# Performance work log

Hardware: AMD Instinct MI355X
Metric: run time of the kernel (lower is better)

The kernel has to match this reference:

```python
import jax, jax.numpy as jnp
import numpy as np

B, S, D = 2, 2048, 1024
H, DH = 16, 64  # num_heads, per-head depth (kd//H == vd//H)
NEG = -1e10


def setup_inputs() -> dict:
    key = jax.random.key(0)
    ks = jax.random.split(key, 5)
    scale = 0.02
    return {
        "X": jax.random.normal(ks[0], (B, S, D), dtype=jnp.float32),
        "Wq": jax.random.normal(ks[1], (D, D), dtype=jnp.float32) * scale,
        "Wk": jax.random.normal(ks[2], (D, D), dtype=jnp.float32) * scale,
        "Wv": jax.random.normal(ks[3], (D, D), dtype=jnp.float32) * scale,
        "Wo": jax.random.normal(ks[4], (D, D), dtype=jnp.float32) * scale,
    }


def reference(X, Wq, Wk, Wv, Wo):
    # torch nn.Linear(in,out,bias=False): y = x @ W.T, W is [out,in]
    q = X @ Wq.T  # [B,S,H*DH]
    k = X @ Wk.T
    v = X @ Wv.T
    # split heads -> [B,H,S,DH]
    q = q.reshape(B, S, H, DH).transpose(0, 2, 1, 3) * (DH ** -0.5)
    k = k.reshape(B, S, H, DH).transpose(0, 2, 1, 3)
    v = v.reshape(B, S, H, DH).transpose(0, 2, 1, 3)
    # causal bias: -1e10 on strictly upper triangle (psuedolikelihood=False)
    bias = NEG * jnp.triu(jnp.ones((S, S), dtype=jnp.float32), 1)
    # logits[...,q,k] = q . k
    logits = jnp.einsum("bhkd,bhqd->bhqk", k, q) + bias
    weights = jax.nn.softmax(logits, axis=-1)  # [B,H,S,S]
    out = jnp.einsum("bhqk,bhkd->bhqd", weights, v)
    out = out.transpose(0, 2, 1, 3).reshape(B, S, H * DH)
    return out @ Wo.T  # [B,S,D]
```

## Files before the change

### kernel.cpp

```cpp
#include <hip/hip_runtime.h>
#include <math.h>


typedef _Float16 f16x8 __attribute__((ext_vector_type(8)));
typedef _Float16 f16x4 __attribute__((ext_vector_type(4)));
typedef _Float16 f16x2 __attribute__((ext_vector_type(2)));
typedef __attribute__((ext_vector_type(4))) float f32x4;
typedef __attribute__((ext_vector_type(16))) float f32x16;

#define MFMA16(a, b, c) __builtin_amdgcn_mfma_f32_16x16x32_f16(a, b, c, 0, 0, 0)
#define MFMA32(a, b, c) __builtin_amdgcn_mfma_f32_32x32x16_f16(a, b, c, 0, 0, 0)
#define QSCALE 0.18033688f

__device__ __forceinline__ void async16(const void* g, void* l) {
  __builtin_amdgcn_global_load_lds(
      (const __attribute__((address_space(1))) unsigned int*)g,
      (__attribute__((address_space(3))) unsigned int*)l, 16, 0, 0);
}

__device__ __forceinline__ f16x2 pk2(float x, float y) {
  return __builtin_bit_cast(f16x2, __builtin_amdgcn_cvt_pkrtz(x, y));
}

__device__ __forceinline__ f16x8 cvt8(const float* __restrict__ p) {
  float4 a = *(const float4*)p;
  float4 b = *(const float4*)(p + 4);
  f16x2 p0 = pk2(a.x, a.y), p1 = pk2(a.z, a.w);
  f16x2 p2 = pk2(b.x, b.y), p3 = pk2(b.z, b.w);
  f16x8 h;
  h[0] = p0[0]; h[1] = p0[1]; h[2] = p1[0]; h[3] = p1[1];
  h[4] = p2[0]; h[5] = p2[1]; h[6] = p3[0]; h[7] = p3[1];
  return h;
}

__global__ void convert_all(const float* __restrict__ X, const float* __restrict__ Wq,
                            const float* __restrict__ Wk, const float* __restrict__ Wv,
                            const float* __restrict__ Wo, _Float16* __restrict__ Xh,
                            _Float16* __restrict__ Wqkvh, _Float16* __restrict__ Woh) {
  size_t i = ((size_t)blockIdx.x * 256 + threadIdx.x) * 8;
  const float* src; _Float16* dst; size_t off;
  if (i < 4194304u)      { src = X;  dst = Xh;              off = i; }
  else if (i < 5242880u) { src = Wq; dst = Wqkvh;           off = i - 4194304u; }
  else if (i < 6291456u) { src = Wk; dst = Wqkvh + 1048576; off = i - 5242880u; }
  else if (i < 7340032u) { src = Wv; dst = Wqkvh + 2097152; off = i - 6291456u; }
  else                   { src = Wo; dst = Woh;             off = i - 7340032u; }
  *(f16x8*)(dst + off) = cvt8(src + off);
}

__global__ __launch_bounds__(256) void gemm_qkv_a(
    const _Float16* __restrict__ Xh, const _Float16* __restrict__ Wh,
    _Float16* __restrict__ Qh, _Float16* __restrict__ Kh,
    _Float16* __restrict__ Vth) {
  __shared__ _Float16 As[128 * 32];
  __shared__ _Float16 Bs[128 * 32];
  const int tid = threadIdx.x;
  const int wave = tid >> 6, lane = tid & 63;
  const int quad = lane >> 4, l16 = lane & 15;
  const int wm = (wave >> 1) * 64, wn = (wave & 1) * 64;
  const int bn = blockIdx.x, bm = blockIdx.y;
  const int mat = bn >> 3;

  const int r0 = tid >> 2, cc0 = (tid & 3) * 8;
  const int r1 = (tid + 256) >> 2, cc1 = (tid & 3) * 8;
  const _Float16* gA0 = &Xh[(size_t)(bm * 128 + r0) * 1024 + cc0];
  const _Float16* gA1 = &Xh[(size_t)(bm * 128 + r1) * 1024 + cc1];
  const _Float16* gB0 = &Wh[(size_t)(bn * 128 + r0) * 1024 + cc0];
  const _Float16* gB1 = &Wh[(size_t)(bn * 128 + r1) * 1024 + cc1];

  f32x4 acc[4][4] = {};

  for (int k0 = 0; k0 < 1024; k0 += 32) {
    __syncthreads();
    async16(gA0 + k0, &As[(wave * 64) * 8]);
    async16(gA1 + k0, &As[(256 + wave * 64) * 8]);
    async16(gB0 + k0, &Bs[(wave * 64) * 8]);
    async16(gB1 + k0, &Bs[(256 + wave * 64) * 8]);
    __syncthreads();
    f16x8 af[4], bf[4];
#pragma unroll
    for (int t = 0; t < 4; ++t) {
      af[t] = *(const f16x8*)&As[(wm + t * 16 + l16) * 32 + quad * 8];
      bf[t] = *(const f16x8*)&Bs[(wn + t * 16 + l16) * 32 + quad * 8];
    }
#pragma unroll
    for (int mt = 0; mt < 4; ++mt)
#pragma unroll
      for (int nt = 0; nt < 4; ++nt)
        acc[mt][nt] = MFMA16(af[mt], bf[nt], acc[mt][nt]);
  }

#pragma unroll
  for (int mt = 0; mt < 4; ++mt) {
    int m_base = bm * 128 + wm + mt * 16 + quad * 4;
    int b = m_base >> 11, sb = m_base & 2047;
#pragma unroll
    for (int nt = 0; nt < 4; ++nt) {
      int ob = (bn * 128 + wn + nt * 16) & 1023;
      int h = ob >> 6;
      int dh = (ob & 63) + l16;
      size_t bh = (size_t)(b * 16 + h);
      if (mat == 0) {
#pragma unroll
        for (int r = 0; r < 4; ++r)
          Qh[(bh * 2048 + sb + r) * 64 + dh] = (_Float16)(acc[mt][nt][r] * QSCALE);
      } else if (mat == 1) {
#pragma unroll
        for (int r = 0; r < 4; ++r)
          Kh[(bh * 2048 + sb + r) * 64 + dh] = (_Float16)acc[mt][nt][r];
      } else {
        f16x4 pk;
        pk[0] = (_Float16)acc[mt][nt][0];
        pk[1] = (_Float16)acc[mt][nt][1];
        pk[2] = (_Float16)acc[mt][nt][2];
        pk[3] = (_Float16)acc[mt][nt][3];
        *(f16x4*)&Vth[(bh * 64 + dh) * 2048 + sb] = pk;
      }
    }
  }
}

__global__ __launch_bounds__(256) void gemm_qkv_f(
    const _Float16* __restrict__ Xh, const float* __restrict__ Wq,
    const float* __restrict__ Wk, const float* __restrict__ Wv,
    _Float16* __restrict__ Qh, _Float16* __restrict__ Kh,
    _Float16* __restrict__ Vth) {
  __shared__ _Float16 As[128 * 72];
  __shared__ _Float16 Bs[128 * 72];
  const int tid = threadIdx.x;
  const int wave = tid >> 6, lane = tid & 63;
  const int quad = lane >> 4, l16 = lane & 15;
  const int wm = (wave >> 1) * 64, wn = (wave & 1) * 64;
  const int bn = blockIdx.x, bm = blockIdx.y;
  const int mat = bn >> 3;
  const float* Bsrc = (mat == 0) ? Wq : (mat == 1) ? Wk : Wv;
  const int brow0 = (bn & 7) * 128;

  f32x4 acc[4][4] = {};

  for (int k0 = 0; k0 < 1024; k0 += 64) {
    __syncthreads();
#pragma unroll
    for (int j = 0; j < 4; ++j) {
      int idx = tid + j * 256;
      int row = idx >> 3, c8 = idx & 7;
      *(int4*)&As[row * 72 + c8 * 8] =
          *(const int4*)&Xh[(size_t)(bm * 128 + row) * 1024 + k0 + c8 * 8];
      *(f16x8*)&Bs[row * 72 + c8 * 8] =
          cvt8(&Bsrc[(size_t)(brow0 + row) * 1024 + k0 + c8 * 8]);
    }
    __syncthreads();
#pragma unroll
    for (int kc = 0; kc < 2; ++kc) {
      f16x8 af[4], bf[4];
#pragma unroll
      for (int t = 0; t < 4; ++t) {
        af[t] = *(const f16x8*)&As[(wm + t * 16 + l16) * 72 + kc * 32 + quad * 8];
        bf[t] = *(const f16x8*)&Bs[(wn + t * 16 + l16) * 72 + kc * 32 + quad * 8];
      }
#pragma unroll
      for (int mt = 0; mt < 4; ++mt)
#pragma unroll
        for (int nt = 0; nt < 4; ++nt)
          acc[mt][nt] = MFMA16(af[mt], bf[nt], acc[mt][nt]);
    }
  }

#pragma unroll
  for (int mt = 0; mt < 4; ++mt) {
    int m_base = bm * 128 + wm + mt * 16 + quad * 4;
    int b = m_base >> 11, sb = m_base & 2047;
#pragma unroll
    for (int nt = 0; nt < 4; ++nt) {
      int ob = (bn * 128 + wn + nt * 16) & 1023;
      int h = ob >> 6;
      int dh = (ob & 63) + l16;
      size_t bh = (size_t)(b * 16 + h);
      if (mat == 0) {
#pragma unroll
        for (int r = 0; r < 4; ++r)
          Qh[(bh * 2048 + sb + r) * 64 + dh] = (_Float16)(acc[mt][nt][r] * QSCALE);
      } else if (mat == 1) {
#pragma unroll
        for (int r = 0; r < 4; ++r)
          Kh[(bh * 2048 + sb + r) * 64 + dh] = (_Float16)acc[mt][nt][r];
      } else {
        f16x4 pk;
        pk[0] = (_Float16)acc[mt][nt][0];
        pk[1] = (_Float16)acc[mt][nt][1];
        pk[2] = (_Float16)acc[mt][nt][2];
        pk[3] = (_Float16)acc[mt][nt][3];
        *(f16x4*)&Vth[(bh * 64 + dh) * 2048 + sb] = pk;
      }
    }
  }
}

__global__ __launch_bounds__(512) void attn_kernel(
    const _Float16* __restrict__ Qg, const _Float16* __restrict__ Kg,
    const _Float16* __restrict__ Vtg, _Float16* __restrict__ Og) {
  __shared__ _Float16 smem[2 * (128 * 72 + 64 * 136)];
  const int bh = blockIdx.x;
  const int qt = 15 - (int)blockIdx.y;
  const int q0 = qt * 128;
  const int tid = threadIdx.x;
  const int group = tid >> 8;
  const int tidg = tid & 255;
  const int wv = (tid >> 6) & 3;
  const int lane = tid & 63;
  const int l31 = lane & 31, hl = lane >> 5;
  const int b = bh >> 4, h = bh & 15;
  const int qrow = q0 + wv * 32 + l31;

  _Float16* Kl = smem + group * (128 * 72 + 64 * 136);
  _Float16* Vl = Kl + 128 * 72;

  const _Float16* Qbase = Qg + ((size_t)bh * 2048 + qrow) * 64 + hl * 8;
  f16x8 aq[4];
#pragma unroll
  for (int t = 0; t < 4; ++t) aq[t] = *(const f16x8*)(Qbase + 16 * t);

  f32x16 oacc[2] = {};
  float la = 0.f, lb = 0.f;

  const int krow = tidg >> 3, kc8 = (tidg & 7) * 8;
  const int vrow = tidg >> 4, vc16 = (tidg & 15) * 8;
  const _Float16* gK = Kg + ((size_t)bh * 2048 + krow) * 64 + kc8;
  const _Float16* gV = Vtg + ((size_t)bh * 64 + vrow) * 2048 + vc16;

  int4 ka0, ka1, ka2, ka3, va0, va1, va2, va3;
  {
    const int ktp = (group <= qt) ? group : qt;
    const _Float16* kp = gK + (size_t)ktp * (128 * 64);
    const _Float16* vp = gV + (size_t)ktp * 128;
    ka0 = *(const int4*)(kp + 0 * 32 * 64);
    ka1 = *(const int4*)(kp + 1 * 32 * 64);
    ka2 = *(const int4*)(kp + 2 * 32 * 64);
    ka3 = *(const int4*)(kp + 3 * 32 * 64);
    va0 = *(const int4*)(vp + 0 * 16 * 2048);
    va1 = *(const int4*)(vp + 1 * 16 * 2048);
    va2 = *(const int4*)(vp + 2 * 16 * 2048);
    va3 = *(const int4*)(vp + 3 * 16 * 2048);
  }

  const int nmax = (qt + 2) >> 1;
  for (int it = 0; it < nmax; ++it) {
    const int kt = 2 * it + group;
    const bool valid = (kt <= qt);
    const int k0 = kt << 7;
    __syncthreads();
    *(int4*)&Kl[(krow + 0) * 72 + kc8] = ka0;
    *(int4*)&Kl[(krow + 32) * 72 + kc8] = ka1;
    *(int4*)&Kl[(krow + 64) * 72 + kc8] = ka2;
    *(int4*)&Kl[(krow + 96) * 72 + kc8] = ka3;
    *(int4*)&Vl[(vrow + 0) * 136 + vc16] = va0;
    *(int4*)&Vl[(vrow + 16) * 136 + vc16] = va1;
    *(int4*)&Vl[(vrow + 32) * 136 + vc16] = va2;
    *(int4*)&Vl[(vrow + 48) * 136 + vc16] = va3;
    {
      const int ktn = (kt + 2 <= qt) ? (kt + 2) : qt;
      const _Float16* kp = gK + (size_t)ktn * (128 * 64);
      const _Float16* vp = gV + (size_t)ktn * 128;
      ka0 = *(const int4*)(kp + 0 * 32 * 64);
      ka1 = *(const int4*)(kp + 1 * 32 * 64);
      ka2 = *(const int4*)(kp + 2 * 32 * 64);
      ka3 = *(const int4*)(kp + 3 * 32 * 64);
      va0 = *(const int4*)(vp + 0 * 16 * 2048);
      va1 = *(const int4*)(vp + 1 * 16 * 2048);
      va2 = *(const int4*)(vp + 2 * 16 * 2048);
      va3 = *(const int4*)(vp + 3 * 16 * 2048);
    }
    __syncthreads();
    if (!valid) continue;

    const bool diag = (kt == qt);

#pragma unroll
    for (int s32t = 0; s32t < 4; ++s32t) {
      if (diag && s32t > wv) break;
      f32x16 tv = {};
      __builtin_amdgcn_s_setprio(1);
#pragma unroll
      for (int t = 0; t < 4; ++t) {
        f16x8 kb = *(const f16x8*)&Kl[(s32t * 32 + l31) * 72 + t * 16 + hl * 8];
        tv = MFMA32(kb, aq[t], tv);
      }
      __builtin_amdgcn_s_setprio(0);
      int pkx[8];
#pragma unroll
      for (int i = 0; i < 8; ++i) {
        float x0 = tv[2 * i], x1 = tv[2 * i + 1];
        int kg = k0 + s32t * 32 + ((2 * i) & 3) + 8 * (i >> 1) + 4 * hl;
        if (diag) {
          if (kg > qrow) x0 = -1e30f;
          if (kg + 1 > qrow) x1 = -1e30f;
        }
        x0 = __builtin_amdgcn_exp2f(x0);
        x1 = __builtin_amdgcn_exp2f(x1);
        la += x0;
        lb += x1;
        pkx[i] = __builtin_bit_cast(int, pk2(x0, x1));
      }
      int s0 = hl ? pkx[0] : pkx[2];
      int s1 = hl ? pkx[1] : pkx[3];
      int s2 = hl ? pkx[4] : pkx[6];
      int s3 = hl ? pkx[5] : pkx[7];
      int r0 = __shfl_xor(s0, 32);
      int r1 = __shfl_xor(s1, 32);
      int r2 = __shfl_xor(s2, 32);
      int r3 = __shfl_xor(s3, 32);
      int4 f0, f1;
      f0.x = hl ? r0 : pkx[0];
      f0.y = hl ? r1 : pkx[1];
      f0.z = hl ? pkx[2] : r0;
      f0.w = hl ? pkx[3] : r1;
      f1.x = hl ? r2 : pkx[4];
      f1.y = hl ? r3 : pkx[5];
      f1.z = hl ? pkx[6] : r2;
      f1.w = hl ? pkx[7] : r3;
      f16x8 bp0 = __builtin_bit_cast(f16x8, f0);
      f16x8 bp1 = __builtin_bit_cast(f16x8, f1);
      __builtin_amdgcn_s_setprio(1);
#pragma unroll
      for (int d = 0; d < 2; ++d) {
        f16x8 vb0 = *(const f16x8*)&Vl[(d * 32 + l31) * 136 + s32t * 32 + hl * 8];
        f16x8 vb1 =
            *(const f16x8*)&Vl[(d * 32 + l31) * 136 + s32t * 32 + 16 + hl * 8];
        oacc[d] = MFMA32(vb0, bp0, oacc[d]);
        oacc[d] = MFMA32(vb1, bp1, oacc[d]);
      }
      __builtin_amdgcn_s_setprio(0);
    }
  }

  float lsum = la + lb;
  __syncthreads();
  float* mbuf = (float*)(smem + (128 * 72 + 64 * 136));
  float* slot = mbuf + (wv * 64 + lane) * 33;
  if (group == 1) {
#pragma unroll
    for (int d = 0; d < 2; ++d)
#pragma unroll
      for (int j = 0; j < 16; ++j) slot[d * 16 + j] = oacc[d][j];
    slot[32] = lsum;
  }
  __syncthreads();
  if (group == 0) {
#pragma unroll
    for (int d = 0; d < 2; ++d)
#pragma unroll
      for (int j = 0; j < 16; ++j) oacc[d][j] += slot[d * 16 + j];
    lsum += slot[32];
    lsum += __shfl_xor(lsum, 32);
    float inv = 1.0f / lsum;
#pragma unroll
    for (int d = 0; d < 2; ++d)
#pragma unroll
      for (int rq = 0; rq < 4; ++rq) {
        f16x4 o;
#pragma unroll
        for (int j = 0; j < 4; ++j)
          o[j] = (_Float16)(oacc[d][rq * 4 + j] * inv);
        int dh = d * 32 + 8 * rq + 4 * hl;
        *(f16x4*)&Og[(((size_t)b * 2048 + qrow) * 16 + h) * 64 + dh] = o;
      }
  }
}

__global__ __launch_bounds__(256) void gemm_out_a(
    const _Float16* __restrict__ A, const _Float16* __restrict__ Woh,
    float* __restrict__ Co) {
  __shared__ _Float16 As[128 * 32];
  __shared__ _Float16 Bs[64 * 32];
  const int tid = threadIdx.x;
  const int wave = tid >> 6, lane = tid & 63;
  const int quad = lane >> 4, l16 = lane & 15;
  const int wm = (wave >> 1) * 64, wn = (wave & 1) * 32;
  const int bn = blockIdx.x, bm = blockIdx.y;

  const int r0 = tid >> 2, cc0 = (tid & 3) * 8;
  const int r1 = (tid + 256) >> 2;
  const _Float16* gA0 = &A[(size_t)(bm * 128 + r0) * 1024 + cc0];
  const _Float16* gA1 = &A[(size_t)(bm * 128 + r1) * 1024 + cc0];
  const _Float16* gB0 = &Woh[(size_t)(bn * 64 + r0) * 1024 + cc0];

  f32x4 acc[4][2] = {};

  for (int k0 = 0; k0 < 1024; k0 += 32) {
    __syncthreads();
    async16(gA0 + k0, &As[(wave * 64) * 8]);
    async16(gA1 + k0, &As[(256 + wave * 64) * 8]);
    if (r0 < 64) async16(gB0 + k0, &Bs[(wave * 64) * 8]);
    __syncthreads();
    f16x8 af[4], bf[2];
#pragma unroll
    for (int t = 0; t < 4; ++t)
      af[t] = *(const f16x8*)&As[(wm + t * 16 + l16) * 32 + quad * 8];
#pragma unroll
    for (int t = 0; t < 2; ++t)
      bf[t] = *(const f16x8*)&Bs[(wn + t * 16 + l16) * 32 + quad * 8];
#pragma unroll
    for (int mt = 0; mt < 4; ++mt)
#pragma unroll
      for (int nt = 0; nt < 2; ++nt)
        acc[mt][nt] = MFMA16(af[mt], bf[nt], acc[mt][nt]);
  }

#pragma unroll
  for (int mt = 0; mt < 4; ++mt) {
    int m_base = bm * 128 + wm + mt * 16 + quad * 4;
#pragma unroll
    for (int nt = 0; nt < 2; ++nt) {
      int n = bn * 64 + wn + nt * 16 + l16;
#pragma unroll
      for (int r = 0; r < 4; ++r)
        Co[(size_t)(m_base + r) * 1024 + n] = acc[mt][nt][r];
    }
  }
}

__global__ __launch_bounds__(256) void gemm_out_f(
    const _Float16* __restrict__ A, const float* __restrict__ Wo,
    float* __restrict__ Co) {
  __shared__ _Float16 As[128 * 72];
  __shared__ _Float16 Bs[64 * 72];
  const int tid = threadIdx.x;
  const int wave = tid >> 6, lane = tid & 63;
  const int quad = lane >> 4, l16 = lane & 15;
  const int wm = (wave >> 1) * 64, wn = (wave & 1) * 32;
  const int bn = blockIdx.x, bm = blockIdx.y;

  f32x4 acc[4][2] = {};

  for (int k0 = 0; k0 < 1024; k0 += 64) {
    __syncthreads();
#pragma unroll
    for (int j = 0; j < 4; ++j) {
      int idx = tid + j * 256;
      int row = idx >> 3, c8 = idx & 7;
      *(int4*)&As[row * 72 + c8 * 8] =
          *(const int4*)&A[(size_t)(bm * 128 + row) * 1024 + k0 + c8 * 8];
    }
#pragma unroll
    for (int j = 0; j < 2; ++j) {
      int idx = tid + j * 256;
      int row = idx >> 3, c8 = idx & 7;
      *(f16x8*)&Bs[row * 72 + c8 * 8] =
          cvt8(&Wo[(size_t)(bn * 64 + row) * 1024 + k0 + c8 * 8]);
    }
    __syncthreads();
#pragma unroll
    for (int kc = 0; kc < 2; ++kc) {
      f16x8 af[4], bf[2];
#pragma unroll
      for (int t = 0; t < 4; ++t)
        af[t] = *(const f16x8*)&As[(wm + t * 16 + l16) * 72 + kc * 32 + quad * 8];
#pragma unroll
      for (int t = 0; t < 2; ++t)
        bf[t] = *(const f16x8*)&Bs[(wn + t * 16 + l16) * 72 + kc * 32 + quad * 8];
#pragma unroll
      for (int mt = 0; mt < 4; ++mt)
#pragma unroll
        for (int nt = 0; nt < 2; ++nt)
          acc[mt][nt] = MFMA16(af[mt], bf[nt], acc[mt][nt]);
    }
  }

#pragma unroll
  for (int mt = 0; mt < 4; ++mt) {
    int m_base = bm * 128 + wm + mt * 16 + quad * 4;
#pragma unroll
    for (int nt = 0; nt < 2; ++nt) {
      int n = bn * 64 + wn + nt * 16 + l16;
#pragma unroll
      for (int r = 0; r < 4; ++r)
        Co[(size_t)(m_base + r) * 1024 + n] = acc[mt][nt][r];
    }
  }
}

extern "C" void kernel_launch(void* const* d_in, const int* in_sizes, int n_in,
                              void* d_out, int out_size, void* d_ws, size_t ws_size,
                              hipStream_t stream) {
  const float* X  = (const float*)d_in[0];
  const float* Wq = (const float*)d_in[1];
  const float* Wk = (const float*)d_in[2];
  const float* Wv = (const float*)d_in[3];
  const float* Wo = (const float*)d_in[4];
  float* out = (float*)d_out;

  _Float16* Qh    = (_Float16*)d_out;
  _Float16* Kh    = Qh + 4194304;
  _Float16* Vth   = (_Float16*)d_ws;
  _Float16* Xh    = Vth + 4194304;
  _Float16* Og    = Xh;
  _Float16* Wqkvh = Xh + 4194304;
  _Float16* Woh   = Wqkvh + 3145728;

  const bool big = (ws_size >= 25165824u);

  convert_all<<<big ? 4096 : 2048, 256, 0, stream>>>(X, Wq, Wk, Wv, Wo,
                                                     Xh, Wqkvh, Woh);
  if (big)
    gemm_qkv_a<<<dim3(24, 32), 256, 0, stream>>>(Xh, Wqkvh, Qh, Kh, Vth);
  else
    gemm_qkv_f<<<dim3(24, 32), 256, 0, stream>>>(Xh, Wq, Wk, Wv, Qh, Kh, Vth);
  attn_kernel<<<dim3(32, 16), 512, 0, stream>>>(Qh, Kh, Vth, Og);
  if (big)
    gemm_out_a<<<dim3(16, 32), 256, 0, stream>>>(Og, Woh, out);
  else
    gemm_out_f<<<dim3(16, 32), 256, 0, stream>>>(Og, Wo, out);
}
```

Before: 177.0 us.

## Fuse conversion+QKV and attention+output projection into persistent kernels with grid barriers

Replaces the four-kernel pipeline with two persistent kernels. One converts the inputs and then runs the QKV GEMM. The other runs attention and then the output projection. Each pair of stages is separated by an atomic-counter grid barrier, which removes launch gaps and inter-kernel drain. Each attention block now handles a causal tile pair (j, 511-j) to balance the work. The exchange is an extra memset, spin-wait barriers that need every block to be co-resident, and a slightly larger workspace requirement for the fast path.

```diff
diff --git a/kernel.cpp b/kernel.cpp
--- a/kernel.cpp
+++ b/kernel.cpp
@@ -33,11 +33,27 @@
   return h;
 }
 
-__global__ void convert_all(const float* __restrict__ X, const float* __restrict__ Wq,
-                            const float* __restrict__ Wk, const float* __restrict__ Wv,
-                            const float* __restrict__ Wo, _Float16* __restrict__ Xh,
-                            _Float16* __restrict__ Wqkvh, _Float16* __restrict__ Woh) {
-  size_t i = ((size_t)blockIdx.x * 256 + threadIdx.x) * 8;
+__device__ __forceinline__ void gbar(unsigned* cnt, unsigned* flag,
+                                     unsigned nblk) {
+  __syncthreads();
+  if (threadIdx.x == 0) {
+    __threadfence();
+    unsigned prev = atomicAdd(cnt, 1u);
+    if (prev + 1 == nblk) {
+      atomicExch(flag, 1u);
+    } else {
+      while (atomicAdd(flag, 0u) == 0u) __builtin_amdgcn_s_sleep(2);
+    }
+    __threadfence();
+  }
+  __syncthreads();
+}
+
+__device__ __forceinline__ void cvt_chunk(
+    size_t i, const float* __restrict__ X, const float* __restrict__ Wq,
+    const float* __restrict__ Wk, const float* __restrict__ Wv,
+    const float* __restrict__ Wo, _Float16* __restrict__ Xh,
+    _Float16* __restrict__ Wqkvh, _Float16* __restrict__ Woh) {
   const float* src; _Float16* dst; size_t off;
   if (i < 4194304u)      { src = X;  dst = Xh;              off = i; }
   else if (i < 5242880u) { src = Wq; dst = Wqkvh;           off = i - 4194304u; }
@@ -47,25 +63,27 @@
   *(f16x8*)(dst + off) = cvt8(src + off);
 }
 
-__global__ __launch_bounds__(256) void gemm_qkv_a(
-    const _Float16* __restrict__ Xh, const _Float16* __restrict__ Wh,
-    _Float16* __restrict__ Qh, _Float16* __restrict__ Kh,
-    _Float16* __restrict__ Vth) {
-  __shared__ _Float16 As[128 * 32];
-  __shared__ _Float16 Bs[128 * 32];
+__global__ void convert_all(const float* __restrict__ X, _Float16* __restrict__ Xh) {
+  size_t i = ((size_t)blockIdx.x * 256 + threadIdx.x) * 8;
+  *(f16x8*)(Xh + i) = cvt8(X + i);
+}
+
+__device__ __forceinline__ void qkv_body(
+    _Float16* As, _Float16* Bs, const _Float16* __restrict__ Xh,
+    const _Float16* __restrict__ Wh, _Float16* __restrict__ Qh,
+    _Float16* __restrict__ Kh, _Float16* __restrict__ Vth, int bn, int bm) {
   const int tid = threadIdx.x;
   const int wave = tid >> 6, lane = tid & 63;
   const int quad = lane >> 4, l16 = lane & 15;
   const int wm = (wave >> 1) * 64, wn = (wave & 1) * 64;
-  const int bn = blockIdx.x, bm = blockIdx.y;
   const int mat = bn >> 3;
 
   const int r0 = tid >> 2, cc0 = (tid & 3) * 8;
-  const int r1 = (tid + 256) >> 2, cc1 = (tid & 3) * 8;
+  const int r1 = (tid + 256) >> 2;
   const _Float16* gA0 = &Xh[(size_t)(bm * 128 + r0) * 1024 + cc0];
-  const _Float16* gA1 = &Xh[(size_t)(bm * 128 + r1) * 1024 + cc1];
+  const _Float16* gA1 = &Xh[(size_t)(bm * 128 + r1) * 1024 + cc0];
   const _Float16* gB0 = &Wh[(size_t)(bn * 128 + r0) * 1024 + cc0];
-  const _Float16* gB1 = &Wh[(size_t)(bn * 128 + r1) * 1024 + cc1];
+  const _Float16* gB1 = &Wh[(size_t)(bn * 128 + r1) * 1024 + cc0];
 
   f32x4 acc[4][4] = {};
 
@@ -117,6 +135,23 @@
       }
     }
   }
+}
+
+__global__ __launch_bounds__(256, 2) void fused_cvt_qkv(
+    const float* __restrict__ X, const float* __restrict__ Wq,
+    const float* __restrict__ Wk, const float* __restrict__ Wv,
+    const float* __restrict__ Wo, _Float16* __restrict__ Xh,
+    _Float16* __restrict__ Wqkvh, _Float16* __restrict__ Woh,
+    _Float16* __restrict__ Qh, _Float16* __restrict__ Kh,
+    _Float16* __restrict__ Vth, unsigned* bar) {
+  __shared__ _Float16 As[128 * 32];
+  __shared__ _Float16 Bs[128 * 32];
+  const int bx = (int)blockIdx.x;
+  for (unsigned c = bx * 256 + threadIdx.x; c < 1048576u; c += 98304u)
+    cvt_chunk((size_t)c * 8, X, Wq, Wk, Wv, Wo, Xh, Wqkvh, Woh);
+  gbar(bar + 0, bar + 1, 384);
+  qkv_body(As, Bs, Xh, Wqkvh, Qh, Kh, Vth, bx % 24, bx / 24);
+  qkv_body(As, Bs, Xh, Wqkvh, Qh, Kh, Vth, bx % 24, (bx + 384) / 24);
 }
 
 __global__ __launch_bounds__(256) void gemm_qkv_f(
@@ -195,12 +230,10 @@
   }
 }
 
-__global__ __launch_bounds__(512) void attn_kernel(
-    const _Float16* __restrict__ Qg, const _Float16* __restrict__ Kg,
-    const _Float16* __restrict__ Vtg, _Float16* __restrict__ Og) {
-  __shared__ _Float16 smem[2 * (128 * 72 + 64 * 136)];
-  const int bh = blockIdx.x;
-  const int qt = 15 - (int)blockIdx.y;
+__device__ __forceinline__ void attn_body(
+    _Float16* smem, const _Float16* Qg, const _Float16* Kg,
+    const _Float16* __restrict__ Vtg, _Float16* __restrict__ Og,
+    int bh, int qt) {
   const int q0 = qt * 128;
   const int tid = threadIdx.x;
   const int group = tid >> 8;
@@ -366,56 +399,86 @@
   }
 }
 
-__global__ __launch_bounds__(256) void gemm_out_a(
-    const _Float16* __restrict__ A, const _Float16* __restrict__ Woh,
-    float* __restrict__ Co) {
-  __shared__ _Float16 As[128 * 32];
-  __shared__ _Float16 Bs[64 * 32];
+__global__ __launch_bounds__(512) void attn_kernel(
+    const _Float16* __restrict__ Qg, const _Float16* __restrict__ Kg,
+    const _Float16* __restrict__ Vtg, _Float16* __restrict__ Og) {
+  __shared__ _Float16 smem[2 * (128 * 72 + 64 * 136)];
+  attn_body(smem, Qg, Kg, Vtg, Og, (int)blockIdx.x, 15 - (int)blockIdx.y);
+}
+
+__device__ __forceinline__ void out_tile(
+    _Float16* smem, const _Float16* Og, const _Float16* __restrict__ Woh,
+    float* Co, int bn, int bm) {
+  _Float16* As = smem;
+  _Float16* Bs = smem + 128 * 32;
   const int tid = threadIdx.x;
   const int wave = tid >> 6, lane = tid & 63;
   const int quad = lane >> 4, l16 = lane & 15;
   const int wm = (wave >> 1) * 64, wn = (wave & 1) * 32;
-  const int bn = blockIdx.x, bm = blockIdx.y;
-
-  const int r0 = tid >> 2, cc0 = (tid & 3) * 8;
-  const int r1 = (tid + 256) >> 2;
-  const _Float16* gA0 = &A[(size_t)(bm * 128 + r0) * 1024 + cc0];
-  const _Float16* gA1 = &A[(size_t)(bm * 128 + r1) * 1024 + cc0];
+  const bool act = (tid < 256);
+
+  const int r0 = (tid & 255) >> 2, cc0 = (tid & 3) * 8;
+  const int r1 = ((tid & 255) + 256) >> 2;
+  const _Float16* gA0 = &Og[(size_t)(bm * 128 + r0) * 1024 + cc0];
+  const _Float16* gA1 = &Og[(size_t)(bm * 128 + r1) * 1024 + cc0];
   const _Float16* gB0 = &Woh[(size_t)(bn * 64 + r0) * 1024 + cc0];
 
   f32x4 acc[4][2] = {};
 
   for (int k0 = 0; k0 < 1024; k0 += 32) {
     __syncthreads();
-    async16(gA0 + k0, &As[(wave * 64) * 8]);
-    async16(gA1 + k0, &As[(256 + wave * 64) * 8]);
-    if (r0 < 64) async16(gB0 + k0, &Bs[(wave * 64) * 8]);
-    __syncthreads();
-    f16x8 af[4], bf[2];
-#pragma unroll
-    for (int t = 0; t < 4; ++t)
-      af[t] = *(const f16x8*)&As[(wm + t * 16 + l16) * 32 + quad * 8];
-#pragma unroll
-    for (int t = 0; t < 2; ++t)
-      bf[t] = *(const f16x8*)&Bs[(wn + t * 16 + l16) * 32 + quad * 8];
-#pragma unroll
-    for (int mt = 0; mt < 4; ++mt)
-#pragma unroll
-      for (int nt = 0; nt < 2; ++nt)
-        acc[mt][nt] = MFMA16(af[mt], bf[nt], acc[mt][nt]);
-  }
-
-#pragma unroll
-  for (int mt = 0; mt < 4; ++mt) {
-    int m_base = bm * 128 + wm + mt * 16 + quad * 4;
-#pragma unroll
-    for (int nt = 0; nt < 2; ++nt) {
-      int n = bn * 64 + wn + nt * 16 + l16;
-#pragma unroll
-      for (int r = 0; r < 4; ++r)
-        Co[(size_t)(m_base + r) * 1024 + n] = acc[mt][nt][r];
-    }
-  }
+    if (act) {
+      async16(gA0 + k0, &As[(wave * 64) * 8]);
+      async16(gA1 + k0, &As[(256 + wave * 64) * 8]);
+      async16(gB0 + k0, &Bs[(wave * 64) * 8]);
+    }
+    __syncthreads();
+    if (act) {
+      f16x8 af[4], bf[2];
+#pragma unroll
+      for (int t = 0; t < 4; ++t)
+        af[t] = *(const f16x8*)&As[(wm + t * 16 + l16) * 32 + quad * 8];
+#pragma unroll
+      for (int t = 0; t < 2; ++t)
+        bf[t] = *(const f16x8*)&Bs[(wn + t * 16 + l16) * 32 + quad * 8];
+#pragma unroll
+      for (int mt = 0; mt < 4; ++mt)
+#pragma unroll
+        for (int nt = 0; nt < 2; ++nt)
+          acc[mt][nt] = MFMA16(af[mt], bf[nt], acc[mt][nt]);
+    }
+  }
+
+  if (act) {
+#pragma unroll
+    for (int mt = 0; mt < 4; ++mt) {
+      int m_base = bm * 128 + wm + mt * 16 + quad * 4;
+#pragma unroll
+      for (int nt = 0; nt < 2; ++nt) {
+        int n = bn * 64 + wn + nt * 16 + l16;
+#pragma unroll
+        for (int r = 0; r < 4; ++r)
+          Co[(size_t)(m_base + r) * 1024 + n] = acc[mt][nt][r];
+      }
+    }
+  }
+}
+
+__global__ __launch_bounds__(512) void fused_attn_out(
+    const _Float16* Qg, const _Float16* Kg,
+    const _Float16* __restrict__ Vtg, _Float16* __restrict__ Og,
+    const _Float16* __restrict__ Woh, float* Co, unsigned* bar) {
+  __shared__ _Float16 smem[2 * (128 * 72 + 64 * 136)];
+  const int bx = (int)blockIdx.x;
+  {
+    int j1 = bx;
+    attn_body(smem, Qg, Kg, Vtg, Og, j1 & 31, 15 - (j1 >> 5));
+    int j2 = 511 - bx;
+    attn_body(smem, Qg, Kg, Vtg, Og, j2 & 31, 15 - (j2 >> 5));
+  }
+  gbar(bar + 2, bar + 3, 256);
+  out_tile(smem, Og, Woh, Co, bx & 15, bx >> 4);
+  out_tile(smem, Og, Woh, Co, (bx + 256) & 15, (bx + 256) >> 4);
 }
 
 __global__ __launch_bounds__(256) void gemm_out_f(
@@ -495,18 +558,19 @@
   _Float16* Og    = Xh;
   _Float16* Wqkvh = Xh + 4194304;
   _Float16* Woh   = Wqkvh + 3145728;
-
-  const bool big = (ws_size >= 25165824u);
-
-  convert_all<<<big ? 4096 : 2048, 256, 0, stream>>>(X, Wq, Wk, Wv, Wo,
-                                                     Xh, Wqkvh, Woh);
-  if (big)
-    gemm_qkv_a<<<dim3(24, 32), 256, 0, stream>>>(Xh, Wqkvh, Qh, Kh, Vth);
-  else
+  unsigned* bar   = (unsigned*)((char*)d_ws + 25165824);
+
+  const bool big = (ws_size >= 25165824u + 64u);
+
+  if (big) {
+    hipMemsetAsync(bar, 0, 64, stream);
+    fused_cvt_qkv<<<384, 256, 0, stream>>>(X, Wq, Wk, Wv, Wo, Xh, Wqkvh, Woh,
+                                           Qh, Kh, Vth, bar);
+    fused_attn_out<<<256, 512, 0, stream>>>(Qh, Kh, Vth, Og, Woh, out, bar);
+  } else {
+    convert_all<<<2048, 256, 0, stream>>>(X, Xh);
     gemm_qkv_f<<<dim3(24, 32), 256, 0, stream>>>(Xh, Wq, Wk, Wv, Qh, Kh, Vth);
-  attn_kernel<<<dim3(32, 16), 512, 0, stream>>>(Qh, Kh, Vth, Og);
-  if (big)
-    gemm_out_a<<<dim3(16, 32), 256, 0, stream>>>(Og, Woh, out);
-  else
+    attn_kernel<<<dim3(32, 16), 512, 0, stream>>>(Qh, Kh, Vth, Og);
     gemm_out_f<<<dim3(16, 32), 256, 0, stream>>>(Og, Wo, out);
-}
+  }
+}
```

Result: slower. 267.2 us (+51.0%).
